# Optimization experiments

Measured on AMD Instinct MI355X. Metric: run time of the kernel, lower is better.

The kernel has to match this reference:

```python
import jax, jax.numpy as jnp
import numpy as np

TEMPERATURE = 0.1
EPS = 1e-8  # matches torch F.cosine_similarity eps


def setup_inputs() -> dict:
    key = jax.random.key(0)
    feats = jax.random.normal(key, (8192, 256), dtype=jnp.float32)
    return {"feats": feats}


def reference(feats) -> jnp.ndarray:
    n = feats.shape[0]
    # cosine similarity = normalized feats GEMM (avoids O(N^2 D) intermediate)
    norms = jnp.maximum(jnp.linalg.norm(feats, axis=-1, keepdims=True), EPS)
    fn = feats / norms  # [N, D]
    sim = jnp.einsum('nd,md->nm', fn, fn) / TEMPERATURE  # [N, N]
    eye = jnp.eye(n, dtype=bool)
    masked_sim = jnp.where(eye, -jnp.inf, sim)
    lse = jax.nn.logsumexp(masked_sim, axis=-1)  # [N]
    # torch.roll(masked_sim, n//2, 0).diag()[i] == masked_sim[(i - n//2) % n, i]
    idx = jnp.arange(n)
    pos = masked_sim[(idx - n // 2) % n, idx]  # [N]
    loss = lse - pos
    return jnp.mean(loss)
```

## Files before the change

kernel.cpp:

```cpp
#include <hip/hip_runtime.h>
#include <hip/hip_bf16.h>
#include <math.h>

typedef __attribute__((ext_vector_type(4))) float f32x4;

#define N 8192
#define D 256
#define INV_T 10.0f
#define EPSN 1e-8f

__device__ __forceinline__ void async16(void* lds, const void* g) {
  __builtin_amdgcn_global_load_lds(
      (const __attribute__((address_space(1))) void*)g,
      (__attribute__((address_space(3))) void*)lds,
      16, 0, 0);
}

__device__ __forceinline__ float rowsum16(float v) {
  v += __uint_as_float(__builtin_amdgcn_update_dpp(
      0u, __float_as_uint(v), 0x118, 0xf, 0xf, true));
  v += __uint_as_float(__builtin_amdgcn_update_dpp(
      0u, __float_as_uint(v), 0x114, 0xf, 0xf, true));
  v += __uint_as_float(__builtin_amdgcn_update_dpp(
      0u, __float_as_uint(v), 0x112, 0xf, 0xf, true));
  v += __uint_as_float(__builtin_amdgcn_update_dpp(
      0u, __float_as_uint(v), 0x111, 0xf, 0xf, true));
  return v;
}

__global__ __launch_bounds__(256) void normalize_k(const float* __restrict__ feats,
                                                   unsigned char* __restrict__ fn,
                                                   float* __restrict__ rowsum,
                                                   float* __restrict__ out) {
  int row = blockIdx.x * 4 + (threadIdx.x >> 6);
  int lane = threadIdx.x & 63;
  if (threadIdx.x < 4) rowsum[blockIdx.x * 4 + threadIdx.x] = 0.0f;
  if (blockIdx.x == 0 && threadIdx.x == 0) out[0] = 0.0f;
  float4 v = ((const float4*)(feats + (size_t)row * D))[lane];
  float ss = v.x * v.x + v.y * v.y + v.z * v.z + v.w * v.w;
#pragma unroll
  for (int off = 32; off; off >>= 1) ss += __shfl_xor(ss, off, 64);
  float inv = 1.0f / fmaxf(sqrtf(ss), EPSN);
  int w = __builtin_amdgcn_cvt_pk_fp8_f32(v.x * inv, v.y * inv, 0, false);
  w = __builtin_amdgcn_cvt_pk_fp8_f32(v.z * inv, v.w * inv, w, true);
  ((int*)(fn + (size_t)row * D))[lane] = w;
}

__global__ __launch_bounds__(512, 8) void gemm_lse(const unsigned char* __restrict__ fn,
                                                   float* __restrict__ rowsum,
                                                   float* __restrict__ pos) {
  __shared__ unsigned char As[2][8192];
  __shared__ unsigned char Bs[2][8192];
  __shared__ float lrow[128];
  __shared__ float lcol[128];
  int tid = threadIdx.x;
  int wave = tid >> 6, lane = tid & 63;
  int wm = wave >> 2, wn = wave & 3;
  int hi = lane >> 4, lo = lane & 15;

  int b = blockIdx.x;
  int t = (b & 7) * 260 + (b >> 3);
  int bm = (int)((129.0 - sqrt((double)(16641 - 8 * t))) * 0.5);
  int S = bm * (129 - bm) / 2;
  if (t < S) { --bm; S = bm * (129 - bm) / 2; }
  else { int S1 = (bm + 1) * (128 - bm) / 2; if (t >= S1) { ++bm; S = S1; } }
  int bn = bm + (t - S);

  int sr = tid >> 2;
  int sc = (tid & 3) ^ ((sr >> 1) & 3);
  const unsigned char* gsa = fn + (size_t)(bm * 128 + sr) * D + sc * 16;
  const unsigned char* gsb = fn + (size_t)(bn * 128 + sr) * D + sc * 16;
  auto stage = [&](int buf, int kt) {
    async16(&As[buf][tid * 16], gsa + kt * 64);
    async16(&Bs[buf][tid * 16], gsb + kt * 64);
  };

  int offA[4][2], offB[2][2];
#pragma unroll
  for (int m = 0; m < 4; ++m) {
    int R = wm * 64 + m * 16 + lo;
#pragma unroll
    for (int ks = 0; ks < 2; ++ks)
      offA[m][ks] = R * 64 + ((((ks << 1) | (hi >> 1)) ^ ((R >> 1) & 3)) << 4) +
                    ((hi & 1) << 3);
  }
#pragma unroll
  for (int n = 0; n < 2; ++n) {
    int R = wn * 32 + n * 16 + lo;
#pragma unroll
    for (int ks = 0; ks < 2; ++ks)
      offB[n][ks] = R * 64 + ((((ks << 1) | (hi >> 1)) ^ ((R >> 1) & 3)) << 4) +
                    ((hi & 1) << 3);
  }

  f32x4 acc[4][2];
#pragma unroll
  for (int m = 0; m < 4; ++m)
#pragma unroll
    for (int n = 0; n < 2; ++n) acc[m][n] = (f32x4){0.f, 0.f, 0.f, 0.f};

  auto compute = [&](int buf) {
#pragma unroll
    for (int ks = 0; ks < 2; ++ks) {
      long long a[4], bb[2];
#pragma unroll
      for (int m = 0; m < 4; ++m)
        a[m] = *(const long long*)&As[buf][offA[m][ks]];
#pragma unroll
      for (int n = 0; n < 2; ++n)
        bb[n] = *(const long long*)&Bs[buf][offB[n][ks]];
#pragma unroll
      for (int m = 0; m < 4; ++m)
#pragma unroll
        for (int n = 0; n < 2; ++n)
          acc[m][n] = __builtin_amdgcn_mfma_f32_16x16x32_fp8_fp8(
              a[m], bb[n], acc[m][n], 0, 0, 0);
    }
  };

  stage(0, 0);
  stage(1, 1);
  if (tid < 128) { lrow[tid] = 0.0f; lcol[tid] = 0.0f; }

#pragma unroll
  for (int kt = 0; kt < 4; ++kt) {
    if (kt < 3) asm volatile("s_waitcnt vmcnt(2)" ::: "memory");
    else        asm volatile("s_waitcnt vmcnt(0)" ::: "memory");
    __builtin_amdgcn_s_barrier();
    __builtin_amdgcn_sched_barrier(0);
    compute(kt & 1);
    asm volatile("s_waitcnt lgkmcnt(0)" ::: "memory");
    __builtin_amdgcn_sched_barrier(0);
    __builtin_amdgcn_s_barrier();
    if (kt < 2) stage(kt & 1, kt + 2);
  }

  bool isdiag = (bm == bn);
  float ca[2] = {0.f, 0.f};
  int rbase = wm * 64, cbase = wn * 32;
#pragma unroll
  for (int m = 0; m < 4; ++m) {
#pragma unroll
    for (int j = 0; j < 4; ++j) {
      int rloc = rbase + m * 16 + hi * 4 + j;
      float v = 0.f;
#pragma unroll
      for (int n = 0; n < 2; ++n) {
        float e = __expf(fmaf(acc[m][n][j], 10.0f, -10.0f));
        if (isdiag && rloc == cbase + n * 16 + lo) e = 0.f;
        v += e;
        ca[n] += e;
      }
      v = rowsum16(v);
      if (lo == 15) atomicAdd(&lrow[rloc], v);
    }
  }
  if (!isdiag) {
#pragma unroll
    for (int n = 0; n < 2; ++n) {
      float c = ca[n];
      c += __shfl_xor(c, 16, 64);
      c += __shfl_xor(c, 32, 64);
      if (hi == 0) atomicAdd(&lcol[cbase + n * 16 + lo], c);
    }
  }
  if (bn == bm + 32) {
#pragma unroll
    for (int m = 0; m < 4; ++m) {
      int rb = wm * 64 + m * 16;
#pragma unroll
      for (int n = 0; n < 2; ++n) {
        if (rb == wn * 32 + n * 16 && (lo >> 2) == hi) {
          int j = lo & 3;
          f32x4 a = acc[m][n];
          float pv = (j == 0) ? a[0] : (j == 1) ? a[1] : (j == 2) ? a[2] : a[3];
          pv *= INV_T;
          int gr = bm * 128 + rb + lo;
          pos[gr] = pv;
          pos[gr + N / 2] = pv;
        }
      }
    }
  }
  __syncthreads();
  if (tid < 128) {
    atomicAdd(&rowsum[bm * 128 + tid], lrow[tid]);
    if (!isdiag) atomicAdd(&rowsum[bn * 128 + tid], lcol[tid]);
  }
}

__global__ __launch_bounds__(256) void final_k(const float* __restrict__ rowsum,
                                               const float* __restrict__ pos,
                                               float* __restrict__ out) {
  int tid = threadIdx.x;
  int i = blockIdx.x * 256 + tid;
  float s = 10.0f + logf(rowsum[i]) - pos[i];
#pragma unroll
  for (int off = 32; off; off >>= 1) s += __shfl_xor(s, off, 64);
  __shared__ float red[4];
  if ((tid & 63) == 0) red[tid >> 6] = s;
  __syncthreads();
  if (tid == 0)
    atomicAdd(out, (red[0] + red[1] + red[2] + red[3]) * (1.0f / N));
}

extern "C" void kernel_launch(void* const* d_in, const int* in_sizes, int n_in,
                              void* d_out, int out_size, void* d_ws, size_t ws_size,
                              hipStream_t stream) {
  const float* feats = (const float*)d_in[0];
  float* out = (float*)d_out;
  char* ws = (char*)d_ws;
  unsigned char* fn = (unsigned char*)ws;
  float* pos = (float*)(ws + 2 * 1024 * 1024);
  float* rowsum = (float*)(ws + 2 * 1024 * 1024 + 32 * 1024);

  normalize_k<<<N / 4, 256, 0, stream>>>(feats, fn, rowsum, out);
  gemm_lse<<<(64 * 65) / 2, 512, 0, stream>>>(fn, rowsum, pos);
  final_k<<<32, 256, 0, stream>>>(rowsum, pos, out);
}
```

Before: 39.00 us.

## Load full K tiles into LDS at once instead of double-buffered K pipeline

Replaces the 4-step double-buffered K loop with a single bulk async load of the full 128x256 fp8 A and B tiles into 64KB of LDS, then one barrier followed by 8 back-to-back MFMA k-steps. A new XOR swizzle over 16 chunks per row is meant to keep the LDS reads free of bank conflicts. This removes the per-step waitcnt and barrier overhead, but it raises LDS use and lowers the occupancy hint from 8 to 4 blocks per CU. Nothing inside a block now overlaps load with compute, so it relies on other resident blocks to hide memory latency.

```diff
diff --git a/kernel.cpp b/kernel.cpp
--- a/kernel.cpp
+++ b/kernel.cpp
@@ -46,11 +46,11 @@
   ((int*)(fn + (size_t)row * D))[lane] = w;
 }
 
-__global__ __launch_bounds__(512, 8) void gemm_lse(const unsigned char* __restrict__ fn,
+__global__ __launch_bounds__(512, 4) void gemm_lse(const unsigned char* __restrict__ fn,
                                                    float* __restrict__ rowsum,
                                                    float* __restrict__ pos) {
-  __shared__ unsigned char As[2][8192];
-  __shared__ unsigned char Bs[2][8192];
+  __shared__ unsigned char As[128 * 256];
+  __shared__ unsigned char Bs[128 * 256];
   __shared__ float lrow[128];
   __shared__ float lcol[128];
   int tid = threadIdx.x;
@@ -66,32 +66,17 @@
   else { int S1 = (bm + 1) * (128 - bm) / 2; if (t >= S1) { ++bm; S = S1; } }
   int bn = bm + (t - S);
 
-  int sr = tid >> 2;
-  int sc = (tid & 3) ^ ((sr >> 1) & 3);
-  const unsigned char* gsa = fn + (size_t)(bm * 128 + sr) * D + sc * 16;
-  const unsigned char* gsb = fn + (size_t)(bn * 128 + sr) * D + sc * 16;
-  auto stage = [&](int buf, int kt) {
-    async16(&As[buf][tid * 16], gsa + kt * 64);
-    async16(&Bs[buf][tid * 16], gsb + kt * 64);
-  };
-
-  int offA[4][2], offB[2][2];
+  const unsigned char* ga = fn + (size_t)(bm * 128) * D;
+  const unsigned char* gb = fn + (size_t)(bn * 128) * D;
 #pragma unroll
-  for (int m = 0; m < 4; ++m) {
-    int R = wm * 64 + m * 16 + lo;
-#pragma unroll
-    for (int ks = 0; ks < 2; ++ks)
-      offA[m][ks] = R * 64 + ((((ks << 1) | (hi >> 1)) ^ ((R >> 1) & 3)) << 4) +
-                    ((hi & 1) << 3);
+  for (int inst = 0; inst < 4; ++inst) {
+    int d = tid + inst * 512;
+    int r = d >> 4;
+    int c = (d & 15) ^ (r & 15);
+    async16(&As[d * 16], ga + r * D + c * 16);
+    async16(&Bs[d * 16], gb + r * D + c * 16);
   }
-#pragma unroll
-  for (int n = 0; n < 2; ++n) {
-    int R = wn * 32 + n * 16 + lo;
-#pragma unroll
-    for (int ks = 0; ks < 2; ++ks)
-      offB[n][ks] = R * 64 + ((((ks << 1) | (hi >> 1)) ^ ((R >> 1) & 3)) << 4) +
-                    ((hi & 1) << 3);
-  }
+  if (tid < 128) { lrow[tid] = 0.0f; lcol[tid] = 0.0f; }
 
   f32x4 acc[4][2];
 #pragma unroll
@@ -99,40 +84,30 @@
 #pragma unroll
     for (int n = 0; n < 2; ++n) acc[m][n] = (f32x4){0.f, 0.f, 0.f, 0.f};
 
-  auto compute = [&](int buf) {
+  __syncthreads();
+
+  int sub = ((hi & 1) << 3);
+  int rA[4], rB[2];
 #pragma unroll
-    for (int ks = 0; ks < 2; ++ks) {
-      long long a[4], bb[2];
+  for (int m = 0; m < 4; ++m) rA[m] = (wm * 64 + m * 16 + lo) * 256 + sub;
 #pragma unroll
-      for (int m = 0; m < 4; ++m)
-        a[m] = *(const long long*)&As[buf][offA[m][ks]];
+  for (int n = 0; n < 2; ++n) rB[n] = (wn * 32 + n * 16 + lo) * 256 + sub;
+#pragma unroll
+  for (int ks = 0; ks < 8; ++ks) {
+    int ch = ((ks << 1) | (hi >> 1)) ^ lo;
+    long long a[4], bb[2];
+#pragma unroll
+    for (int m = 0; m < 4; ++m)
+      a[m] = *(const long long*)&As[rA[m] + (ch << 4)];
+#pragma unroll
+    for (int n = 0; n < 2; ++n)
+      bb[n] = *(const long long*)&Bs[rB[n] + (ch << 4)];
+#pragma unroll
+    for (int m = 0; m < 4; ++m)
 #pragma unroll
       for (int n = 0; n < 2; ++n)
-        bb[n] = *(const long long*)&Bs[buf][offB[n][ks]];
-#pragma unroll
-      for (int m = 0; m < 4; ++m)
-#pragma unroll
-        for (int n = 0; n < 2; ++n)
-          acc[m][n] = __builtin_amdgcn_mfma_f32_16x16x32_fp8_fp8(
-              a[m], bb[n], acc[m][n], 0, 0, 0);
-    }
-  };
-
-  stage(0, 0);
-  stage(1, 1);
-  if (tid < 128) { lrow[tid] = 0.0f; lcol[tid] = 0.0f; }
-
-#pragma unroll
-  for (int kt = 0; kt < 4; ++kt) {
-    if (kt < 3) asm volatile("s_waitcnt vmcnt(2)" ::: "memory");
-    else        asm volatile("s_waitcnt vmcnt(0)" ::: "memory");
-    __builtin_amdgcn_s_barrier();
-    __builtin_amdgcn_sched_barrier(0);
-    compute(kt & 1);
-    asm volatile("s_waitcnt lgkmcnt(0)" ::: "memory");
-    __builtin_amdgcn_sched_barrier(0);
-    __builtin_amdgcn_s_barrier();
-    if (kt < 2) stage(kt & 1, kt + 2);
+        acc[m][n] = __builtin_amdgcn_mfma_f32_16x16x32_fp8_fp8(
+            a[m], bb[n], acc[m][n], 0, 0, 0);
   }
 
   bool isdiag = (bm == bn);
```

Result: slower. 41.51 us (+6.4%).

## Widen GEMM tile to 128x256 over paired column blocks with MFMA priority

Applied to the files above, without the earlier changes.

Each block now covers one 128-row block against a 256-column pair of blocks. The triangular schedule is remapped to 1056 blocks, and each wave skips its half when it falls below the diagonal. This doubles MFMA work per A-tile load, cuts block count and per-block overhead, and raises wave priority around the MFMA bursts. In exchange it adds wasted compute on diagonal pairs where half the waves idle, more LDS and register use, and lower occupancy (launch bounds 6).

```diff
diff --git a/kernel.cpp b/kernel.cpp
--- a/kernel.cpp
+++ b/kernel.cpp
@@ -46,36 +46,41 @@
   ((int*)(fn + (size_t)row * D))[lane] = w;
 }
 
-__global__ __launch_bounds__(512, 8) void gemm_lse(const unsigned char* __restrict__ fn,
+__global__ __launch_bounds__(512, 6) void gemm_lse(const unsigned char* __restrict__ fn,
                                                    float* __restrict__ rowsum,
                                                    float* __restrict__ pos) {
   __shared__ unsigned char As[2][8192];
-  __shared__ unsigned char Bs[2][8192];
+  __shared__ unsigned char Bs[2][16384];
   __shared__ float lrow[128];
-  __shared__ float lcol[128];
+  __shared__ float lcol[256];
   int tid = threadIdx.x;
   int wave = tid >> 6, lane = tid & 63;
   int wm = wave >> 2, wn = wave & 3;
   int hi = lane >> 4, lo = lane & 15;
 
   int b = blockIdx.x;
-  int t = (b & 7) * 260 + (b >> 3);
-  int bm = (int)((129.0 - sqrt((double)(16641 - 8 * t))) * 0.5);
-  int S = bm * (129 - bm) / 2;
-  if (t < S) { --bm; S = bm * (129 - bm) / 2; }
-  else { int S1 = (bm + 1) * (128 - bm) / 2; if (t >= S1) { ++bm; S = S1; } }
-  int bn = bm + (t - S);
-
-  int sr = tid >> 2;
-  int sc = (tid & 3) ^ ((sr >> 1) & 3);
-  const unsigned char* gsa = fn + (size_t)(bm * 128 + sr) * D + sc * 16;
-  const unsigned char* gsb = fn + (size_t)(bn * 128 + sr) * D + sc * 16;
+  int t = (b & 7) * 132 + (b >> 3);
+  int h = (int)((65.0f - sqrtf((float)(4225 - 4 * t))) * 0.5f);
+  h = h < 0 ? 0 : (h > 31 ? 31 : h);
+  while (t < h * (65 - h)) --h;
+  while (t >= (h + 1) * (64 - h)) ++h;
+  int r = t - h * (65 - h);
+  int bm = 2 * h + (r & 1);
+  int p = h + (r >> 1);
+
+  const unsigned char* ga = fn + (size_t)(bm * 128) * D;
+  const unsigned char* gb = fn + (size_t)(p * 256) * D;
+
+  int da = tid, ra = da >> 2, caa = ((da & 3) ^ ((ra >> 1) & 3)) * 16;
+  int d0 = tid, r0 = d0 >> 2, c0 = ((d0 & 3) ^ ((r0 >> 1) & 3)) * 16;
+  int d1 = tid + 512, r1 = d1 >> 2, c1 = ((d1 & 3) ^ ((r1 >> 1) & 3)) * 16;
   auto stage = [&](int buf, int kt) {
-    async16(&As[buf][tid * 16], gsa + kt * 64);
-    async16(&Bs[buf][tid * 16], gsb + kt * 64);
+    async16(&As[buf][da * 16], ga + (size_t)ra * D + kt * 64 + caa);
+    async16(&Bs[buf][d0 * 16], gb + (size_t)r0 * D + kt * 64 + c0);
+    async16(&Bs[buf][d1 * 16], gb + (size_t)r1 * D + kt * 64 + c1);
   };
 
-  int offA[4][2], offB[2][2];
+  int offA[4][2], offB[4][2];
 #pragma unroll
   for (int m = 0; m < 4; ++m) {
     int R = wm * 64 + m * 16 + lo;
@@ -85,46 +90,49 @@
                     ((hi & 1) << 3);
   }
 #pragma unroll
-  for (int n = 0; n < 2; ++n) {
-    int R = wn * 32 + n * 16 + lo;
+  for (int n = 0; n < 4; ++n) {
+    int R = wn * 64 + n * 16 + lo;
 #pragma unroll
     for (int ks = 0; ks < 2; ++ks)
       offB[n][ks] = R * 64 + ((((ks << 1) | (hi >> 1)) ^ ((R >> 1) & 3)) << 4) +
                     ((hi & 1) << 3);
   }
 
-  f32x4 acc[4][2];
+  f32x4 acc[4][4];
 #pragma unroll
   for (int m = 0; m < 4; ++m)
 #pragma unroll
-    for (int n = 0; n < 2; ++n) acc[m][n] = (f32x4){0.f, 0.f, 0.f, 0.f};
+    for (int n = 0; n < 4; ++n) acc[m][n] = (f32x4){0.f, 0.f, 0.f, 0.f};
 
   auto compute = [&](int buf) {
 #pragma unroll
     for (int ks = 0; ks < 2; ++ks) {
-      long long a[4], bb[2];
+      long long a[4], bb[4];
 #pragma unroll
       for (int m = 0; m < 4; ++m)
         a[m] = *(const long long*)&As[buf][offA[m][ks]];
 #pragma unroll
-      for (int n = 0; n < 2; ++n)
+      for (int n = 0; n < 4; ++n)
         bb[n] = *(const long long*)&Bs[buf][offB[n][ks]];
+      __builtin_amdgcn_s_setprio(1);
 #pragma unroll
       for (int m = 0; m < 4; ++m)
 #pragma unroll
-        for (int n = 0; n < 2; ++n)
+        for (int n = 0; n < 4; ++n)
           acc[m][n] = __builtin_amdgcn_mfma_f32_16x16x32_fp8_fp8(
               a[m], bb[n], acc[m][n], 0, 0, 0);
+      __builtin_amdgcn_s_setprio(0);
     }
   };
 
   stage(0, 0);
   stage(1, 1);
-  if (tid < 128) { lrow[tid] = 0.0f; lcol[tid] = 0.0f; }
+  if (tid < 128) lrow[tid] = 0.0f;
+  if (tid < 256) lcol[tid] = 0.0f;
 
 #pragma unroll
   for (int kt = 0; kt < 4; ++kt) {
-    if (kt < 3) asm volatile("s_waitcnt vmcnt(2)" ::: "memory");
+    if (kt < 3) asm volatile("s_waitcnt vmcnt(3)" ::: "memory");
     else        asm volatile("s_waitcnt vmcnt(0)" ::: "memory");
     __builtin_amdgcn_s_barrier();
     __builtin_amdgcn_sched_barrier(0);
@@ -135,57 +143,62 @@
     if (kt < 2) stage(kt & 1, kt + 2);
   }
 
-  bool isdiag = (bm == bn);
-  float ca[2] = {0.f, 0.f};
-  int rbase = wm * 64, cbase = wn * 32;
-#pragma unroll
-  for (int m = 0; m < 4; ++m) {
-#pragma unroll
-    for (int j = 0; j < 4; ++j) {
-      int rloc = rbase + m * 16 + hi * 4 + j;
-      float v = 0.f;
-#pragma unroll
-      for (int n = 0; n < 2; ++n) {
-        float e = __expf(fmaf(acc[m][n][j], 10.0f, -10.0f));
-        if (isdiag && rloc == cbase + n * 16 + lo) e = 0.f;
-        v += e;
-        ca[n] += e;
+  int bnW = 2 * p + (wn >> 1);
+  bool wvalid = (bnW >= bm);
+  bool isdiag = (bnW == bm);
+  int rbase = wm * 64;
+  int clocal = (wn & 1) * 64;
+  if (wvalid) {
+    float ca[4] = {0.f, 0.f, 0.f, 0.f};
+#pragma unroll
+    for (int m = 0; m < 4; ++m) {
+#pragma unroll
+      for (int j = 0; j < 4; ++j) {
+        int rloc = rbase + m * 16 + hi * 4 + j;
+        float v = 0.f;
+#pragma unroll
+        for (int n = 0; n < 4; ++n) {
+          float e = __expf(fmaf(acc[m][n][j], 10.0f, -10.0f));
+          if (isdiag && rloc == clocal + n * 16 + lo) e = 0.f;
+          v += e;
+          ca[n] += e;
+        }
+        v = rowsum16(v);
+        if (lo == 15) atomicAdd(&lrow[rloc], v);
       }
-      v = rowsum16(v);
-      if (lo == 15) atomicAdd(&lrow[rloc], v);
-    }
-  }
-  if (!isdiag) {
-#pragma unroll
-    for (int n = 0; n < 2; ++n) {
-      float c = ca[n];
-      c += __shfl_xor(c, 16, 64);
-      c += __shfl_xor(c, 32, 64);
-      if (hi == 0) atomicAdd(&lcol[cbase + n * 16 + lo], c);
-    }
-  }
-  if (bn == bm + 32) {
-#pragma unroll
-    for (int m = 0; m < 4; ++m) {
-      int rb = wm * 64 + m * 16;
-#pragma unroll
-      for (int n = 0; n < 2; ++n) {
-        if (rb == wn * 32 + n * 16 && (lo >> 2) == hi) {
-          int j = lo & 3;
-          f32x4 a = acc[m][n];
-          float pv = (j == 0) ? a[0] : (j == 1) ? a[1] : (j == 2) ? a[2] : a[3];
-          pv *= INV_T;
-          int gr = bm * 128 + rb + lo;
-          pos[gr] = pv;
-          pos[gr + N / 2] = pv;
+    }
+    if (!isdiag) {
+#pragma unroll
+      for (int n = 0; n < 4; ++n) {
+        float c = ca[n];
+        c += __shfl_xor(c, 16, 64);
+        c += __shfl_xor(c, 32, 64);
+        if (hi == 0) atomicAdd(&lcol[wn * 64 + n * 16 + lo], c);
+      }
+    }
+    if (bnW == bm + 32) {
+#pragma unroll
+      for (int m = 0; m < 4; ++m) {
+#pragma unroll
+        for (int n = 0; n < 4; ++n) {
+          if (wm * 64 + m * 16 == clocal + n * 16 && (lo >> 2) == hi) {
+            int j = lo & 3;
+            f32x4 a = acc[m][n];
+            float pv = (j == 0) ? a[0] : (j == 1) ? a[1] : (j == 2) ? a[2] : a[3];
+            pv *= INV_T;
+            int gr = bm * 128 + wm * 64 + m * 16 + lo;
+            pos[gr] = pv;
+            pos[gr + N / 2] = pv;
+          }
         }
       }
     }
   }
   __syncthreads();
-  if (tid < 128) {
-    atomicAdd(&rowsum[bm * 128 + tid], lrow[tid]);
-    if (!isdiag) atomicAdd(&rowsum[bn * 128 + tid], lcol[tid]);
+  if (tid < 128) atomicAdd(&rowsum[bm * 128 + tid], lrow[tid]);
+  if (tid < 256) {
+    int bnX = 2 * p + (tid >> 7);
+    if (bnX > bm) atomicAdd(&rowsum[bnX * 128 + (tid & 127)], lcol[tid]);
   }
 }
 
@@ -215,6 +228,6 @@
   float* rowsum = (float*)(ws + 2 * 1024 * 1024 + 32 * 1024);
 
   normalize_k<<<N / 4, 256, 0, stream>>>(feats, fn, rowsum, out);
-  gemm_lse<<<(64 * 65) / 2, 512, 0, stream>>>(fn, rowsum, pos);
+  gemm_lse<<<1056, 512, 0, stream>>>(fn, rowsum, pos);
   final_k<<<32, 256, 0, stream>>>(rowsum, pos, out);
 }
```

New measurement: 75.06 us. 1.92x slower.
